# Performance work log

Measured on AMD Instinct MI355X. Metric: run time of the kernel, lower is better.

The kernel has to match this reference:

```python
import jax, jax.numpy as jnp
import numpy as np

B, N, C, H = 1, 4096, 512, 8
S = 64  # sqrt(N), static


def setup_inputs() -> dict:
    key = jax.random.key(0)
    ks = jax.random.split(key, 4)
    d = C // H
    return {
        "x": jax.random.normal(ks[0], (B, N, C), dtype=jnp.float32),
        "num_heads": H,
        "bias": jnp.zeros((1,), dtype=jnp.float32),  # unused in original forward
        "scale": jnp.asarray(d ** -0.5, dtype=jnp.float32),
        "Wqkv": jax.random.normal(ks[1], (3 * C, C), dtype=jnp.float32) * (C ** -0.5),
        "bqkv": jnp.zeros((3 * C,), dtype=jnp.float32),
        "Wproj": jax.random.normal(ks[2], (C, C), dtype=jnp.float32) * (C ** -0.5),
        "bproj": jnp.zeros((C,), dtype=jnp.float32),
    }


def reference(x, num_heads, bias, scale, Wqkv, bqkv, Wproj, bproj):
    b, n, c = x.shape
    d = c // num_heads
    # fused QKV projection: [b, n, 3c] -> [3, b, h, n, d]
    qkv = (x @ Wqkv.T + bqkv).reshape(b, n, 3, num_heads, d).transpose(2, 0, 3, 1, 4)
    q, k, v = qkv[0] * scale, qkv[1], qkv[2]
    attn = jax.nn.softmax(jnp.einsum("bhnd,bhmd->bhnm", q, k), axis=-1)
    out = jnp.einsum("bhnm,bhmd->bhnd", attn, v)
    out = out.transpose(0, 2, 1, 3).reshape(b, n, c)
    out = out @ Wproj.T + bproj
    return out.reshape(b, S, S, c)
```

## Files before the change

kernel.cpp:

```cpp
#include <hip/hip_runtime.h>
#include <stdint.h>

#define NTOK 4096
#define CDIM 512
#define HEADS 8
#define DHEAD 64
#define PHEAD (NTOK * DHEAD)

typedef __bf16 bf16x8 __attribute__((ext_vector_type(8)));
typedef float f32x4 __attribute__((ext_vector_type(4)));

typedef const __attribute__((address_space(1))) unsigned int* gas_ptr;
typedef __attribute__((address_space(3))) unsigned int* las_ptr;

__device__ __forceinline__ unsigned short bfbits(float f) {
    return __builtin_bit_cast(unsigned short, (__bf16)f);
}

__device__ __forceinline__ f32x4 mfma32(bf16x8 a, bf16x8 b, f32x4 c) {
    return __builtin_amdgcn_mfma_f32_16x16x32_bf16(a, b, c, 0, 0, 0);
}

__device__ __forceinline__ void gload16(const unsigned short* g, unsigned short* l) {
    __builtin_amdgcn_global_load_lds((gas_ptr)g, (las_ptr)l, 16, 0, 0);
}

__device__ __forceinline__ void cvt_store8(unsigned short* dst, float4 v0, float4 v1) {
    unsigned short o[8];
    o[0] = bfbits(v0.x); o[1] = bfbits(v0.y); o[2] = bfbits(v0.z); o[3] = bfbits(v0.w);
    o[4] = bfbits(v1.x); o[5] = bfbits(v1.y); o[6] = bfbits(v1.z); o[7] = bfbits(v1.w);
    *(uint4*)dst = *(const uint4*)o;
}

__global__ __launch_bounds__(256) void cast3_k(
    const float* __restrict__ x, const float* __restrict__ wq, const float* __restrict__ wp,
    unsigned short* __restrict__ xb, unsigned short* __restrict__ wqb,
    unsigned short* __restrict__ wpb)
{
    const int b = blockIdx.x;
    const float* src; unsigned short* dst; int off;
    if (b < 1024)      { src = x;  dst = xb;  off = b; }
    else if (b < 1408) { src = wq; dst = wqb; off = b - 1024; }
    else               { src = wp; dst = wpb; off = b - 1408; }
    const int i = (off * 256 + threadIdx.x) * 8;
    const float4 v0 = *(const float4*)(src + i);
    const float4 v1 = *(const float4*)(src + i + 4);
    cvt_store8(dst + i, v0, v1);
}

__global__ __launch_bounds__(256) void gemm_qkv(
    const unsigned short* __restrict__ A,
    const unsigned short* __restrict__ Bm,
    const float* __restrict__ bias,
    const float* __restrict__ scale_p,
    unsigned short* __restrict__ qkv_out)
{
    __shared__ __align__(16) unsigned short smem[2 * 6144];

    const int tid = threadIdx.x;
    const int mBase = blockIdx.y * 64, nBase = blockIdx.x * 128;
    const int lane = tid & 63;
    const int w = __builtin_amdgcn_readfirstlane(tid >> 6);
    const int l16 = lane & 15, quad = lane >> 4;

    const unsigned short* gA  = &A[(size_t)(mBase + (tid >> 2)) * CDIM + (tid & 3) * 8];
    const unsigned short* gB0 = &Bm[(size_t)(nBase + (tid >> 2)) * CDIM + (tid & 3) * 8];
    const unsigned short* gB1 = &Bm[(size_t)(nBase + 64 + (tid >> 2)) * CDIM + (tid & 3) * 8];

    f32x4 acc[4][2] = {};

    gload16(gA, &smem[tid * 8]);
    gload16(gB0, &smem[2048 + tid * 8]);
    gload16(gB1, &smem[4096 + tid * 8]);

    int cur = 0;
    for (int kt = 0; kt < CDIM; kt += 32) {
        __syncthreads();
        if (kt + 32 < CDIM) {
            const int nb = (cur ^ 1) * 6144;
            gload16(gA + kt + 32, &smem[nb + tid * 8]);
            gload16(gB0 + kt + 32, &smem[nb + 2048 + tid * 8]);
            gload16(gB1 + kt + 32, &smem[nb + 4096 + tid * 8]);
        }
        const unsigned short* lA = &smem[cur * 6144];
        const unsigned short* lB = &smem[cur * 6144 + 2048];

        bf16x8 af[4], bfr[2];
#pragma unroll
        for (int i = 0; i < 4; ++i)
            af[i] = *(const bf16x8*)&lA[(i * 16 + l16) * 32 + quad * 8];
#pragma unroll
        for (int j = 0; j < 2; ++j)
            bfr[j] = *(const bf16x8*)&lB[(w * 32 + j * 16 + l16) * 32 + quad * 8];
#pragma unroll
        for (int i = 0; i < 4; ++i)
#pragma unroll
            for (int j = 0; j < 2; ++j)
                acc[i][j] = mfma32(af[i], bfr[j], acc[i][j]);
        cur ^= 1;
    }

    const int three = nBase >> 9;
    const float scl = scale_p[0] * 1.44269504f;
    const float mul = (three == 0) ? scl : 1.0f;

    __syncthreads();
#pragma unroll
    for (int i = 0; i < 4; ++i)
#pragma unroll
        for (int j = 0; j < 2; ++j)
#pragma unroll
            for (int r = 0; r < 4; ++r) {
                const int rl = i * 16 + quad * 4 + r;
                const int cl = w * 32 + j * 16 + l16;
                const float v = (acc[i][j][r] + bias[nBase + cl]) * mul;
                smem[rl * 136 + cl] = bfbits(v);
            }
    __syncthreads();

    const size_t base3 = (size_t)three * (PHEAD * HEADS);
    if (three < 2) {
#pragma unroll
        for (int pass = 0; pass < 4; ++pass) {
            const int idx = pass * 256 + tid;
            const int rl16 = idx & 15, qc = (idx >> 4) & 7;
            const int hsel = (idx >> 7) & 1, t16l = (idx >> 8) & 3;
            const uint4 d = *(const uint4*)&smem[(t16l * 16 + rl16) * 136 + hsel * 64 + qc * 8];
            const int hh = ((nBase >> 6) + hsel) & 7;
            const int t16 = (mBase >> 4) + t16l;
            const size_t dst = base3 + (size_t)hh * PHEAD +
                (size_t)(((t16 * 2 + (qc >> 2)) * 64 + (qc & 3) * 16 + rl16) * 8);
            *(uint4*)&qkv_out[dst] = d;
        }
    } else {
#pragma unroll
        for (int pass = 0; pass < 4; ++pass) {
            const int idx = pass * 256 + tid;
            const int l16t = idx & 15, quadt = (idx >> 4) & 3;
            const int dt = (idx >> 6) & 3, k32l = (idx >> 8) & 1, hsel = (idx >> 9) & 1;
            const int col = hsel * 64 + dt * 16 + l16t;
            unsigned short o8[8];
#pragma unroll
            for (int e = 0; e < 4; ++e) {
                o8[e]     = smem[(k32l * 32 + quadt * 4 + e) * 136 + col];
                o8[e + 4] = smem[(k32l * 32 + 16 + quadt * 4 + e) * 136 + col];
            }
            const int hh = ((nBase >> 6) + hsel) & 7;
            const int k32 = (mBase >> 5) + k32l;
            const size_t dst = base3 + (size_t)hh * PHEAD +
                (size_t)(((k32 * 4 + dt) * 64 + quadt * 16 + l16t) * 8);
            *(uint4*)&qkv_out[dst] = *(uint4*)o8;
        }
    }
}

__global__ __launch_bounds__(256, 2) void flash10_k(
    const unsigned short* __restrict__ qf,
    const unsigned short* __restrict__ kf,
    const unsigned short* __restrict__ vf,
    unsigned short* __restrict__ attn_out)
{
    __shared__ float ldsO[4][64][68];
    __shared__ float sml[4][64];

    const int tid = threadIdx.x;
    const int lane = tid & 63;
    const int w = __builtin_amdgcn_readfirstlane(tid >> 6);
    const int l16 = lane & 15, quad = lane >> 4;
    const int h = blockIdx.x, qb = blockIdx.y;

    const unsigned short* qh = qf + (size_t)h * PHEAD;
    const unsigned short* kb = kf + (size_t)h * PHEAD + w * 65536;
    const unsigned short* vb = vf + (size_t)h * PHEAD + w * 65536;

    bf16x8 qfr[4][2];
#pragma unroll
    for (int qt = 0; qt < 4; ++qt)
#pragma unroll
        for (int d2 = 0; d2 < 2; ++d2)
            qfr[qt][d2] = *(const bf16x8*)&qh[((qb * 4 + qt) * 2 + d2) * 512 + lane * 8];

    f32x4 oacc[4][4] = {};
    float lv[4] = {};

    bf16x8 k0[4], k1[4], v0[4], v1[4];
    f32x4 s[4][2];
    bf16x8 pf[4];

    auto LK = [&](bf16x8* dst, int t) {
#pragma unroll
        for (int i = 0; i < 4; ++i)
            dst[i] = *(const bf16x8*)&kb[t * 2048 + i * 512 + lane * 8];
    };
    auto LV = [&](bf16x8* dst, int t) {
#pragma unroll
        for (int i = 0; i < 4; ++i)
            dst[i] = *(const bf16x8*)&vb[t * 2048 + i * 512 + lane * 8];
    };
    auto QK = [&](bf16x8* ku) {
#pragma unroll
        for (int qt = 0; qt < 4; ++qt) {
            f32x4 a = {};
            a = mfma32(ku[0], qfr[qt][0], a);
            a = mfma32(ku[1], qfr[qt][1], a);
            s[qt][0] = a;
            f32x4 b = {};
            b = mfma32(ku[2], qfr[qt][0], b);
            b = mfma32(ku[3], qfr[qt][1], b);
            s[qt][1] = b;
        }
    };
    auto SM = [&]() {
#pragma unroll
        for (int qt = 0; qt < 4; ++qt) {
            float e0[4], e1[4];
#pragma unroll
            for (int r = 0; r < 4; ++r) {
                e0[r] = __builtin_amdgcn_exp2f(s[qt][0][r]);
                e1[r] = __builtin_amdgcn_exp2f(s[qt][1][r]);
            }
            lv[qt] += ((e0[0] + e0[1]) + (e0[2] + e0[3])) +
                      ((e1[0] + e1[1]) + (e1[2] + e1[3]));
            bf16x8 pb;
#pragma unroll
            for (int r = 0; r < 4; ++r) {
                pb[r]     = (__bf16)e0[r];
                pb[4 + r] = (__bf16)e1[r];
            }
            pf[qt] = pb;
        }
    };
    auto PV = [&](bf16x8* vu) {
#pragma unroll
        for (int dt = 0; dt < 4; ++dt)
#pragma unroll
            for (int qt = 0; qt < 4; ++qt)
                oacc[dt][qt] = mfma32(vu[dt], pf[qt], oacc[dt][qt]);
    };

    LK(k0, 0); LV(v0, 0); LK(k1, 1);
    QK(k0);

    for (int ii = 0; ii < 15; ++ii) {
        const int i = ii * 2 + 1;
        LK(k0, i + 1);
        LV(v1, i);
        SM();
        __builtin_amdgcn_s_setprio(1);
        QK(k1);
        PV(v0);
        __builtin_amdgcn_s_setprio(0);
        LK(k1, i + 2);
        LV(v0, i + 1);
        SM();
        __builtin_amdgcn_s_setprio(1);
        QK(k0);
        PV(v1);
        __builtin_amdgcn_s_setprio(0);
    }
    LV(v1, 31);
    SM();
    __builtin_amdgcn_s_setprio(1);
    QK(k1);
    PV(v0);
    __builtin_amdgcn_s_setprio(0);
    SM();
    PV(v1);

#pragma unroll
    for (int qt = 0; qt < 4; ++qt) {
        float L = lv[qt];
        L += __shfl_xor(L, 16, 64);
        L += __shfl_xor(L, 32, 64);
        if (quad == 0) sml[w][qt * 16 + l16] = L;
    }
#pragma unroll
    for (int qt = 0; qt < 4; ++qt) {
        const int q = qt * 16 + l16;
#pragma unroll
        for (int dt = 0; dt < 4; ++dt)
            *(f32x4*)&ldsO[w][q][dt * 16 + quad * 4] = oacc[dt][qt];
    }
    __syncthreads();
#pragma unroll
    for (int pass = 0; pass < 2; ++pass) {
        const int idx = pass * 256 + tid;
        const int q = idx >> 3, dseg = (idx & 7) * 8;
        const float L = sml[0][q] + sml[1][q] + sml[2][q] + sml[3][q];
        const float inv = 1.f / L;
        unsigned short o8[8];
#pragma unroll
        for (int i = 0; i < 8; ++i) {
            const float v = ldsO[0][q][dseg + i] + ldsO[1][q][dseg + i] +
                            ldsO[2][q][dseg + i] + ldsO[3][q][dseg + i];
            o8[i] = bfbits(v * inv);
        }
        *(uint4*)&attn_out[(size_t)(qb * 64 + q) * CDIM + h * DHEAD + dseg] = *(uint4*)o8;
    }
}

__global__ __launch_bounds__(256) void gemm_proj(
    const unsigned short* __restrict__ A,
    const unsigned short* __restrict__ Bm,
    const float* __restrict__ bias,
    float* __restrict__ c_out)
{
    __shared__ __align__(16) unsigned short smem[2 * 4096];

    const int tid = threadIdx.x;
    const int mBase = blockIdx.y * 64, nBase = blockIdx.x * 64;
    const int lane = tid & 63;
    const int w = __builtin_amdgcn_readfirstlane(tid >> 6);
    const int l16 = lane & 15, quad = lane >> 4;

    const unsigned short* gA = &A[(size_t)(mBase + (tid >> 2)) * CDIM + (tid & 3) * 8];
    const unsigned short* gB = &Bm[(size_t)(nBase + (tid >> 2)) * CDIM + (tid & 3) * 8];

    f32x4 acc[4] = {};

    gload16(gA, &smem[tid * 8]);
    gload16(gB, &smem[2048 + tid * 8]);

    int cur = 0;
    for (int kt = 0; kt < CDIM; kt += 32) {
        __syncthreads();
        if (kt + 32 < CDIM) {
            const int nb = (cur ^ 1) * 4096;
            gload16(gA + kt + 32, &smem[nb + tid * 8]);
            gload16(gB + kt + 32, &smem[nb + 2048 + tid * 8]);
        }
        const unsigned short* lA = &smem[cur * 4096];
        const unsigned short* lB = &smem[cur * 4096 + 2048];

        bf16x8 af[4], bfr;
#pragma unroll
        for (int i = 0; i < 4; ++i)
            af[i] = *(const bf16x8*)&lA[(i * 16 + l16) * 32 + quad * 8];
        bfr = *(const bf16x8*)&lB[(w * 16 + l16) * 32 + quad * 8];
#pragma unroll
        for (int i = 0; i < 4; ++i)
            acc[i] = mfma32(af[i], bfr, acc[i]);
        cur ^= 1;
    }

#pragma unroll
    for (int i = 0; i < 4; ++i)
#pragma unroll
        for (int r = 0; r < 4; ++r) {
            const int grow = mBase + i * 16 + quad * 4 + r;
            const int gcol = nBase + w * 16 + l16;
            c_out[(size_t)grow * CDIM + gcol] = acc[i][r] + bias[gcol];
        }
}

extern "C" void kernel_launch(void* const* d_in, const int* in_sizes, int n_in,
                              void* d_out, int out_size, void* d_ws, size_t ws_size,
                              hipStream_t stream) {
    const float* x       = (const float*)d_in[0];
    const float* scale_p = (const float*)d_in[3];
    const float* Wqkv    = (const float*)d_in[4];
    const float* bqkv    = (const float*)d_in[5];
    const float* Wproj   = (const float*)d_in[6];
    const float* bproj   = (const float*)d_in[7];
    float* out = (float*)d_out;

    char* ws = (char*)d_ws;
    const size_t OFF_QKV  = 0;
    const size_t OFF_ATTN = 12582912;
    const size_t OFF_XB   = 16777216;
    const size_t OFF_WQB  = 20971520;
    const size_t OFF_WPB  = 22544384;
    const size_t NEEDED   = OFF_WPB + 524288;
    if (ws_size < NEEDED) return;

    unsigned short* qkvb  = (unsigned short*)(ws + OFF_QKV);
    unsigned short* attnb = (unsigned short*)(ws + OFF_ATTN);
    unsigned short* xb    = (unsigned short*)(ws + OFF_XB);
    unsigned short* wqb   = (unsigned short*)(ws + OFF_WQB);
    unsigned short* wpb   = (unsigned short*)(ws + OFF_WPB);

    cast3_k<<<1536, 256, 0, stream>>>(x, Wqkv, Wproj, xb, wqb, wpb);

    gemm_qkv<<<dim3(12, 64), 256, 0, stream>>>(xb, wqb, bqkv, scale_p, qkvb);

    const unsigned short* qfr = qkvb;
    const unsigned short* kfr = qkvb + (size_t)PHEAD * HEADS;
    const unsigned short* vfr = qkvb + (size_t)2 * PHEAD * HEADS;
    flash10_k<<<dim3(8, 64), 256, 0, stream>>>(qfr, kfr, vfr, attnb);

    gemm_proj<<<dim3(8, 64), 256, 0, stream>>>(attnb, wpb, bproj, out);
}
```

Before: 147.9 us.

## Swizzle GEMM LDS tiles and reorder flash softmax pipeline

In both GEMM kernels, the global-to-LDS loads now place each row's 16-byte chunks at XOR-swizzled columns, and the fragment reads use the matching swizzled offsets. This is meant to cut LDS bank conflicts on the MFMA operand reads. The flash attention main loop is also reordered so the softmax of one tile runs after the QK/PV MFMA block instead of before it, changing how exp/ALU work overlaps with matrix ops and loads. Both changes alter only scheduling and layout, and correctness depends on the swizzle being applied identically on the store and load sides.

```diff
diff --git a/kernel.cpp b/kernel.cpp
--- a/kernel.cpp
+++ b/kernel.cpp
@@ -63,9 +63,13 @@
     const int w = __builtin_amdgcn_readfirstlane(tid >> 6);
     const int l16 = lane & 15, quad = lane >> 4;
 
-    const unsigned short* gA  = &A[(size_t)(mBase + (tid >> 2)) * CDIM + (tid & 3) * 8];
-    const unsigned short* gB0 = &Bm[(size_t)(nBase + (tid >> 2)) * CDIM + (tid & 3) * 8];
-    const unsigned short* gB1 = &Bm[(size_t)(nBase + 64 + (tid >> 2)) * CDIM + (tid & 3) * 8];
+    const int srow = tid >> 2;
+    const int scol = ((tid & 3) ^ ((tid >> 3) & 3)) * 8;
+    const unsigned short* gA  = &A[(size_t)(mBase + srow) * CDIM + scol];
+    const unsigned short* gB0 = &Bm[(size_t)(nBase + srow) * CDIM + scol];
+    const unsigned short* gB1 = &Bm[(size_t)(nBase + 64 + srow) * CDIM + scol];
+
+    const int qs = (quad ^ ((l16 >> 1) & 3)) * 8;
 
     f32x4 acc[4][2] = {};
 
@@ -88,10 +92,10 @@
         bf16x8 af[4], bfr[2];
 #pragma unroll
         for (int i = 0; i < 4; ++i)
-            af[i] = *(const bf16x8*)&lA[(i * 16 + l16) * 32 + quad * 8];
+            af[i] = *(const bf16x8*)&lA[(i * 16 + l16) * 32 + qs];
 #pragma unroll
         for (int j = 0; j < 2; ++j)
-            bfr[j] = *(const bf16x8*)&lB[(w * 32 + j * 16 + l16) * 32 + quad * 8];
+            bfr[j] = *(const bf16x8*)&lB[(w * 32 + j * 16 + l16) * 32 + qs];
 #pragma unroll
         for (int i = 0; i < 4; ++i)
 #pragma unroll
@@ -154,7 +158,7 @@
     }
 }
 
-__global__ __launch_bounds__(256, 2) void flash10_k(
+__global__ __launch_bounds__(256, 2) void flash12_k(
     const unsigned short* __restrict__ qf,
     const unsigned short* __restrict__ kf,
     const unsigned short* __restrict__ vf,
@@ -183,7 +187,7 @@
     f32x4 oacc[4][4] = {};
     float lv[4] = {};
 
-    bf16x8 k0[4], k1[4], v0[4], v1[4];
+    bf16x8 kA[4], kB[4], vA[4], vB[4];
     f32x4 s[4][2];
     bf16x8 pf[4];
 
@@ -238,34 +242,36 @@
                 oacc[dt][qt] = mfma32(vu[dt], pf[qt], oacc[dt][qt]);
     };
 
-    LK(k0, 0); LV(v0, 0); LK(k1, 1);
-    QK(k0);
-
-    for (int ii = 0; ii < 15; ++ii) {
-        const int i = ii * 2 + 1;
-        LK(k0, i + 1);
-        LV(v1, i);
+    LK(kA, 0);
+    QK(kA);
+    SM();
+    LV(vA, 0);
+    LK(kB, 1);
+
+    for (int it = 0; it < 15; ++it) {
+        const int g = it * 2 + 1;
+        LK(kA, g + 1);
+        LV(vB, g);
+        __builtin_amdgcn_s_setprio(1);
+        QK(kB);
+        PV(vA);
+        __builtin_amdgcn_s_setprio(0);
         SM();
+        LK(kB, g + 2);
+        LV(vA, g + 1);
         __builtin_amdgcn_s_setprio(1);
-        QK(k1);
-        PV(v0);
+        QK(kA);
+        PV(vB);
         __builtin_amdgcn_s_setprio(0);
-        LK(k1, i + 2);
-        LV(v0, i + 1);
         SM();
-        __builtin_amdgcn_s_setprio(1);
-        QK(k0);
-        PV(v1);
-        __builtin_amdgcn_s_setprio(0);
-    }
-    LV(v1, 31);
-    SM();
+    }
+    LV(vB, 31);
     __builtin_amdgcn_s_setprio(1);
-    QK(k1);
-    PV(v0);
+    QK(kB);
+    PV(vA);
     __builtin_amdgcn_s_setprio(0);
     SM();
-    PV(v1);
+    PV(vB);
 
 #pragma unroll
     for (int qt = 0; qt < 4; ++qt) {
@@ -313,8 +319,12 @@
     const int w = __builtin_amdgcn_readfirstlane(tid >> 6);
     const int l16 = lane & 15, quad = lane >> 4;
 
-    const unsigned short* gA = &A[(size_t)(mBase + (tid >> 2)) * CDIM + (tid & 3) * 8];
-    const unsigned short* gB = &Bm[(size_t)(nBase + (tid >> 2)) * CDIM + (tid & 3) * 8];
+    const int srow = tid >> 2;
+    const int scol = ((tid & 3) ^ ((tid >> 3) & 3)) * 8;
+    const unsigned short* gA = &A[(size_t)(mBase + srow) * CDIM + scol];
+    const unsigned short* gB = &Bm[(size_t)(nBase + srow) * CDIM + scol];
+
+    const int qs = (quad ^ ((l16 >> 1) & 3)) * 8;
 
     f32x4 acc[4] = {};
 
@@ -335,8 +345,8 @@
         bf16x8 af[4], bfr;
 #pragma unroll
         for (int i = 0; i < 4; ++i)
-            af[i] = *(const bf16x8*)&lA[(i * 16 + l16) * 32 + quad * 8];
-        bfr = *(const bf16x8*)&lB[(w * 16 + l16) * 32 + quad * 8];
+            af[i] = *(const bf16x8*)&lA[(i * 16 + l16) * 32 + qs];
+        bfr = *(const bf16x8*)&lB[(w * 16 + l16) * 32 + qs];
 #pragma unroll
         for (int i = 0; i < 4; ++i)
             acc[i] = mfma32(af[i], bfr, acc[i]);
@@ -386,7 +396,7 @@
     const unsigned short* qfr = qkvb;
     const unsigned short* kfr = qkvb + (size_t)PHEAD * HEADS;
     const unsigned short* vfr = qkvb + (size_t)2 * PHEAD * HEADS;
-    flash10_k<<<dim3(8, 64), 256, 0, stream>>>(qfr, kfr, vfr, attnb);
+    flash12_k<<<dim3(8, 64), 256, 0, stream>>>(qfr, kfr, vfr, attnb);
 
     gemm_proj<<<dim3(8, 64), 256, 0, stream>>>(attnb, wpb, bproj, out);
 }
```

New measurement: 129.0 us, median of 2. -12.8%, faster.
